# Performance work log

Hardware: AMD Instinct MI355X
Metric: run time of the kernel (lower is better)

Reference implementation:

```python
import jax, jax.numpy as jnp
import numpy as np
from jax import lax

TEMPERATURE = 0.5
MOMENTUM = 0.9
EPS = 1e-12  # F.normalize eps

B, D, K = 8192, 512, 16384


def _l2norm(x):
    # matches F.normalize(p=2): x / max(||x||, eps)
    n = jnp.sqrt(jnp.sum(x * x, axis=-1, keepdims=True))
    return x / jnp.maximum(n, EPS)


def setup_inputs() -> dict:
    key = jax.random.key(0)
    k1, k2, k3 = jax.random.split(key, 3)
    embeddings = jax.random.normal(k1, (B, D), dtype=jnp.float32)
    cluster_ids = jax.random.randint(k2, (B,), 0, K, dtype=jnp.int64)
    prototypes = jax.random.normal(k3, (K, D), dtype=jnp.float32)
    return {"embeddings": embeddings, "cluster_ids": cluster_ids, "prototypes": prototypes}


def reference(embeddings, cluster_ids, prototypes):
    emb_n = _l2norm(embeddings)            # [B, D]
    proto_n = _l2norm(prototypes)          # [K, D]
    sim = jnp.einsum('bd,kd->bk', emb_n, proto_n) / TEMPERATURE  # [B, K]

    pos = jnp.take_along_axis(sim, cluster_ids[:, None], axis=1)  # [B, 1]
    # mask out the positive column, then stable logsumexp over negatives
    is_pos = jnp.arange(sim.shape[1])[None, :] == cluster_ids[:, None]  # [B, K]
    neg = jnp.where(is_pos, -jnp.inf, sim)
    lse = jax.scipy.special.logsumexp(neg, axis=1, keepdims=True)       # [B, 1]
    loss = jnp.mean(-pos + lse)

    # serial momentum EMA update (order-dependent for duplicate cluster ids)
    def step(protos, xc):
        x, c = xc
        row = MOMENTUM * protos[c] + (1.0 - MOMENTUM) * x
        return protos.at[c].set(row), None

    new_protos, _ = lax.scan(step, prototypes, (embeddings, cluster_ids))
    return loss, new_protos
```

## Files before the change

kernel.cpp:

```cpp
#include <hip/hip_runtime.h>
#include <hip/hip_bf16.h>


#define B_N 8192
#define D_N 512
#define K_N 16384
#define INV_T 2.0f
#define MOM 0.9f

#define BM 128
#define BN 128
#define SPLIT 32
#define TILES ((K_N / SPLIT) / BN)
#define CHUNKS (D_N / 128)
#define CAP 64

typedef __attribute__((ext_vector_type(8))) int intx8;
typedef __attribute__((ext_vector_type(16))) float floatx16;

__device__ __forceinline__ void gl_lds16(const void* g, void* lds) {
    __builtin_amdgcn_global_load_lds(
        (const __attribute__((address_space(1))) void*)g,
        (__attribute__((address_space(3))) void*)lds, 16, 0, 0);
}

__global__ void head_kernel(const float* __restrict__ emb, const float* __restrict__ pro,
                            const int* __restrict__ cid,
                            unsigned char* __restrict__ embq, unsigned char* __restrict__ proq,
                            float* __restrict__ rowpos, float* __restrict__ rowsum,
                            float* __restrict__ out, int* __restrict__ cnt) {
    int bx = blockIdx.x;
    int t = threadIdx.x;
    int lane = t & 63;
    if (bx < (B_N + K_N) / 4) {
        if (bx < 32) rowsum[bx * 256 + t] = 0.0f;
        if (bx == 32 && t == 0) out[0] = 0.0f;
        int row = bx * 4 + (t >> 6);
        const float* x;
        unsigned char* o;
        if (row < B_N) {
            x = emb + (size_t)row * D_N;
            o = embq + (size_t)row * D_N;
        } else {
            x = pro + (size_t)(row - B_N) * D_N;
            o = proq + (size_t)(row - B_N) * D_N;
        }
        const float4* xp = (const float4*)(x + lane * 8);
        float4 v0 = xp[0];
        float4 v1 = xp[1];
        float ss = v0.x * v0.x + v0.y * v0.y + v0.z * v0.z + v0.w * v0.w +
                   v1.x * v1.x + v1.y * v1.y + v1.z * v1.z + v1.w * v1.w;
        #pragma unroll
        for (int of = 32; of; of >>= 1) ss += __shfl_xor(ss, of);
        float sc = 16.0f / fmaxf(sqrtf(ss), 1e-12f);
        int w0 = 0, w1 = 0;
        w0 = __builtin_amdgcn_cvt_pk_fp8_f32(v0.x * sc, v0.y * sc, w0, false);
        w0 = __builtin_amdgcn_cvt_pk_fp8_f32(v0.z * sc, v0.w * sc, w0, true);
        w1 = __builtin_amdgcn_cvt_pk_fp8_f32(v1.x * sc, v1.y * sc, w1, false);
        w1 = __builtin_amdgcn_cvt_pk_fp8_f32(v1.z * sc, v1.w * sc, w1, true);
        int2 st = {w0, w1};
        *(int2*)(o + lane * 8) = st;
    } else {
        int pb = bx - (B_N + K_N) / 4;
        if (t < 8) cnt[pb * 8 + t] = 0;
        int b = pb * 4 + (t >> 6);
        int c = cid[b];
        const float4* ep = (const float4*)(emb + (size_t)b * D_N + lane * 8);
        const float4* pp = (const float4*)(pro + (size_t)c * D_N + lane * 8);
        float4 e0 = ep[0], e1 = ep[1], p0 = pp[0], p1 = pp[1];
        float dp = e0.x * p0.x + e0.y * p0.y + e0.z * p0.z + e0.w * p0.w +
                   e1.x * p1.x + e1.y * p1.y + e1.z * p1.z + e1.w * p1.w;
        float ee = e0.x * e0.x + e0.y * e0.y + e0.z * e0.z + e0.w * e0.w +
                   e1.x * e1.x + e1.y * e1.y + e1.z * e1.z + e1.w * e1.w;
        float qq = p0.x * p0.x + p0.y * p0.y + p0.z * p0.z + p0.w * p0.w +
                   p1.x * p1.x + p1.y * p1.y + p1.z * p1.z + p1.w * p1.w;
        #pragma unroll
        for (int o = 32; o; o >>= 1) {
            dp += __shfl_xor(dp, o);
            ee += __shfl_xor(ee, o);
            qq += __shfl_xor(qq, o);
        }
        if (lane == 0)
            rowpos[b] = INV_T * dp / (fmaxf(sqrtf(ee), 1e-12f) * fmaxf(sqrtf(qq), 1e-12f));
    }
}

__global__ __launch_bounds__(256) void flash_kernel(const unsigned char* __restrict__ embq,
                                                    const unsigned char* __restrict__ proq,
                                                    float* __restrict__ rowsum_g) {
    __shared__ __align__(16) unsigned char As[BM * 128];
    __shared__ __align__(16) unsigned char Bs[BN * 128];
    const int t = threadIdx.x;
    const int w = t >> 6, lane = t & 63;
    const int m = lane & 31, q2 = lane >> 5;
    const int wm = w >> 1, wn = w & 1;
    const int rowBase = blockIdx.x * BM;
    const int nBegin = blockIdx.y * (K_N / SPLIT);

    const int e = (m >> 1) & 3;
    const int s0 = (((q2 << 1) | 0) ^ e) << 4;
    const int s1 = s0 ^ 16;
    const unsigned char* aR = &As[(wm * 64 + m) * 64];
    const unsigned char* bR = &Bs[(wn * 64 + m) * 64];

    const unsigned char* aSrcP[4];
    const unsigned char* bSrcP[4];
    #pragma unroll
    for (int p = 0; p < 4; p++) {
        int f = p * 256 + t;
        int r = (f >> 2) & 127;
        int h = f >> 9;
        int g = (f & 3) ^ ((r >> 1) & 3);
        aSrcP[p] = embq + (size_t)(rowBase + r) * D_N + h * 64 + g * 16;
        bSrcP[p] = proq + (size_t)(nBegin + r) * D_N + h * 64 + g * 16;
    }

    float rowsum[32];
    #pragma unroll
    for (int i = 0; i < 32; i++) rowsum[i] = 0.0f;

    #pragma unroll
    for (int p = 0; p < 4; p++) {
        gl_lds16(aSrcP[p], &As[p * 4096 + w * 1024]);
        gl_lds16(bSrcP[p], &Bs[p * 4096 + w * 1024]);
    }

    for (int tile = 0; tile < TILES; tile++) {
        floatx16 acc[2][2];
        #pragma unroll
        for (int mt = 0; mt < 2; mt++)
            #pragma unroll
            for (int nt = 0; nt < 2; nt++)
                #pragma unroll
                for (int r = 0; r < 16; r++) acc[mt][nt][r] = 0.0f;
        #pragma unroll
        for (int ch = 0; ch < CHUNKS; ch++) {
            __syncthreads();
            intx8 af[2][2], bf[2][2];
            #pragma unroll
            for (int mt = 0; mt < 2; mt++)
                #pragma unroll
                for (int h = 0; h < 2; h++) {
                    int4 lo = *(const int4*)(aR + mt * 2048 + h * 8192 + s0);
                    int4 hi = *(const int4*)(aR + mt * 2048 + h * 8192 + s1);
                    intx8 v = {lo.x, lo.y, lo.z, lo.w, hi.x, hi.y, hi.z, hi.w};
                    af[mt][h] = v;
                }
            #pragma unroll
            for (int nt = 0; nt < 2; nt++)
                #pragma unroll
                for (int h = 0; h < 2; h++) {
                    int4 lo = *(const int4*)(bR + nt * 2048 + h * 8192 + s0);
                    int4 hi = *(const int4*)(bR + nt * 2048 + h * 8192 + s1);
                    intx8 v = {lo.x, lo.y, lo.z, lo.w, hi.x, hi.y, hi.z, hi.w};
                    bf[nt][h] = v;
                }
            __syncthreads();
            if (ch + 1 < CHUNKS) {
                #pragma unroll
                for (int p = 0; p < 4; p++) {
                    gl_lds16(aSrcP[p] + (ch + 1) * 128, &As[p * 4096 + w * 1024]);
                    gl_lds16(bSrcP[p] + (ch + 1) * 128, &Bs[p * 4096 + w * 1024]);
                }
            } else if (tile + 1 < TILES) {
                #pragma unroll
                for (int p = 0; p < 4; p++) {
                    gl_lds16(aSrcP[p], &As[p * 4096 + w * 1024]);
                    gl_lds16(bSrcP[p] + (size_t)BN * D_N, &Bs[p * 4096 + w * 1024]);
                }
            }
            #pragma unroll
            for (int mt = 0; mt < 2; mt++)
                #pragma unroll
                for (int nt = 0; nt < 2; nt++)
                    #pragma unroll
                    for (int h = 0; h < 2; h++)
                        acc[mt][nt] = __builtin_amdgcn_mfma_scale_f32_32x32x64_f8f6f4(
                            af[mt][h], bf[nt][h], acc[mt][nt], 0, 0, 0, 0x7F7F7F7F, 0,
                            0x7F7F7F7F);
        }
        #pragma unroll
        for (int p = 0; p < 4; p++) bSrcP[p] += (size_t)BN * D_N;
        #pragma unroll
        for (int mt = 0; mt < 2; mt++)
            #pragma unroll
            for (int nt = 0; nt < 2; nt++)
                #pragma unroll
                for (int r = 0; r < 16; r++)
                    rowsum[mt * 16 + r] += __expf(acc[mt][nt][r] * (INV_T / 256.0f));
    }
    #pragma unroll
    for (int i = 0; i < 32; i++) {
        #pragma unroll
        for (int o = 1; o < 32; o <<= 1) rowsum[i] += __shfl_xor(rowsum[i], o);
    }
    if (m == 0) {
        #pragma unroll
        for (int mt = 0; mt < 2; mt++)
            #pragma unroll
            for (int r = 0; r < 16; r++)
                atomicAdd(&rowsum_g[rowBase + wm * 64 + mt * 32 + (r & 3) + 8 * (r >> 2) +
                                    4 * q2],
                          rowsum[mt * 16 + r]);
    }
}

__global__ void loss_kernel(const float* __restrict__ rowsum, const float* __restrict__ rowpos,
                            float* __restrict__ out) {
    __shared__ float red[256];
    int t = threadIdx.x;
    int b = blockIdx.x * 256 + t;
    float p = rowpos[b];
    red[t] = logf(rowsum[b] - __expf(p)) - p;
    __syncthreads();
    for (int o = 128; o; o >>= 1) {
        if (t < o) red[t] += red[t + o];
        __syncthreads();
    }
    if (t == 0) atomicAdd(out, red[0] * (1.0f / (float)B_N));
}

__global__ void ema_count(const int* __restrict__ cid, int* __restrict__ cnt,
                          int* __restrict__ bucket) {
    int b = blockIdx.x * 256 + threadIdx.x;
    int c = cid[b];
    int slot = atomicAdd(&cnt[c], 1);
    if (slot < CAP) bucket[c * CAP + slot] = b;
}

__global__ void ema_apply(const float* __restrict__ emb, const float* __restrict__ pro,
                          const int* __restrict__ cnt, const int* __restrict__ bucket,
                          float* __restrict__ outp) {
    int k = blockIdx.x * 4 + (threadIdx.x >> 6);
    int lane = threadIdx.x & 63;
    int n = cnt[k];
    n = n < CAP ? n : CAP;
    const float4* pp = (const float4*)(pro + (size_t)k * D_N + lane * 8);
    float4 a0 = pp[0], a1 = pp[1];
    int myb = (lane < n) ? bucket[k * CAP + lane] : 0x7fffffff;
    for (int i = 0; i < n; i++) {
        int m = myb;
        #pragma unroll
        for (int o = 1; o < 64; o <<= 1) {
            int v = __shfl_xor(m, o);
            m = v < m ? v : m;
        }
        const float4* ep = (const float4*)(emb + (size_t)m * D_N + lane * 8);
        float4 e0 = ep[0], e1 = ep[1];
        a0.x = MOM * a0.x + (1.0f - MOM) * e0.x;
        a0.y = MOM * a0.y + (1.0f - MOM) * e0.y;
        a0.z = MOM * a0.z + (1.0f - MOM) * e0.z;
        a0.w = MOM * a0.w + (1.0f - MOM) * e0.w;
        a1.x = MOM * a1.x + (1.0f - MOM) * e1.x;
        a1.y = MOM * a1.y + (1.0f - MOM) * e1.y;
        a1.z = MOM * a1.z + (1.0f - MOM) * e1.z;
        a1.w = MOM * a1.w + (1.0f - MOM) * e1.w;
        if (myb == m) myb = 0x7fffffff;
    }
    float4* op = (float4*)(outp + (size_t)k * D_N + lane * 8);
    op[0] = a0;
    op[1] = a1;
}

extern "C" void kernel_launch(void* const* d_in, const int* in_sizes, int n_in,
                              void* d_out, int out_size, void* d_ws, size_t ws_size,
                              hipStream_t stream) {
    const float* emb = (const float*)d_in[0];
    const int* cid = (const int*)d_in[1];
    const float* pro = (const float*)d_in[2];
    float* out = (float*)d_out;

    char* ws = (char*)d_ws;
    unsigned char* embq = (unsigned char*)ws;
    unsigned char* proq = (unsigned char*)(ws + 4194304);
    float* rowsum = (float*)(ws + 12582912);
    float* rowpos = (float*)(ws + 12615680);
    int* cnt = (int*)(ws + 12648448);
    int* bucket = (int*)(ws + 12713984);

    head_kernel<<<(B_N + K_N) / 4 + B_N / 4, 256, 0, stream>>>(emb, pro, cid, embq, proq,
                                                               rowpos, rowsum, out, cnt);
    ema_count<<<B_N / 256, 256, 0, stream>>>(cid, cnt, bucket);
    flash_kernel<<<dim3(B_N / BM, SPLIT), 256, 0, stream>>>(embq, proq, rowsum);
    loss_kernel<<<B_N / 256, 256, 0, stream>>>(rowsum, rowpos, out);
    ema_apply<<<K_N / 4, 256, 0, stream>>>(emb, pro, cnt, bucket, out + 1);
}
```

Baseline: 214.6 us.

## Restructure FP8 flash GEMM with 16x16x128 MFMA, register B operands, and merged tail kernel

The similarity GEMM kernel is reorganised. The row tile doubles to 256, A tiles are double-buffered in LDS, and B (prototype) fragments are loaded straight from global memory into registers instead of staged through LDS. It switches from 32x32x64 to 16x16x128 scaled FP8 MFMA with an 8x4 accumulator tile per wave. The loss reduction and EMA apply kernels are merged into one launch to save a kernel launch. Risks: B is no longer shared through LDS, so global traffic rises and loads may be uncoalesced, and the larger accumulator set raises register pressure.

```diff
diff --git a/kernel.cpp b/kernel.cpp
--- a/kernel.cpp
+++ b/kernel.cpp
@@ -8,15 +8,13 @@
 #define INV_T 2.0f
 #define MOM 0.9f
 
-#define BM 128
+#define BM 256
 #define BN 128
 #define SPLIT 32
-#define TILES ((K_N / SPLIT) / BN)
-#define CHUNKS (D_N / 128)
 #define CAP 64
 
 typedef __attribute__((ext_vector_type(8))) int intx8;
-typedef __attribute__((ext_vector_type(16))) float floatx16;
+typedef __attribute__((ext_vector_type(4))) float floatx4;
 
 __device__ __forceinline__ void gl_lds16(const void* g, void* lds) {
     __builtin_amdgcn_global_load_lds(
@@ -88,136 +86,107 @@
 __global__ __launch_bounds__(256) void flash_kernel(const unsigned char* __restrict__ embq,
                                                     const unsigned char* __restrict__ proq,
                                                     float* __restrict__ rowsum_g) {
-    __shared__ __align__(16) unsigned char As[BM * 128];
-    __shared__ __align__(16) unsigned char Bs[BN * 128];
+    __shared__ __align__(16) unsigned char As[2][BM * 128];
     const int t = threadIdx.x;
     const int w = t >> 6, lane = t & 63;
-    const int m = lane & 31, q2 = lane >> 5;
+    const int quad = lane >> 4, lcol = lane & 15;
     const int wm = w >> 1, wn = w & 1;
     const int rowBase = blockIdx.x * BM;
     const int nBegin = blockIdx.y * (K_N / SPLIT);
 
-    const int e = (m >> 1) & 3;
-    const int s0 = (((q2 << 1) | 0) ^ e) << 4;
+    const int srow = t >> 3;
+    const int sG = ((t & 7) ^ (srow & 7)) << 4;
+    const unsigned char* aSrc = embq + (size_t)(rowBase + srow) * D_N + sG;
+
+    const int s0 = ((quad << 1) ^ (lcol & 7)) << 4;
     const int s1 = s0 ^ 16;
-    const unsigned char* aR = &As[(wm * 64 + m) * 64];
-    const unsigned char* bR = &Bs[(wn * 64 + m) * 64];
-
-    const unsigned char* aSrcP[4];
-    const unsigned char* bSrcP[4];
-    #pragma unroll
-    for (int p = 0; p < 4; p++) {
-        int f = p * 256 + t;
-        int r = (f >> 2) & 127;
-        int h = f >> 9;
-        int g = (f & 3) ^ ((r >> 1) & 3);
-        aSrcP[p] = embq + (size_t)(rowBase + r) * D_N + h * 64 + g * 16;
-        bSrcP[p] = proq + (size_t)(nBegin + r) * D_N + h * 64 + g * 16;
-    }
+    const int aRow = (wm * 128 + lcol) * 128;
+
+    const unsigned char* bPtr = proq + (size_t)(nBegin + wn * 64 + lcol) * D_N + quad * 32;
 
     float rowsum[32];
     #pragma unroll
     for (int i = 0; i < 32; i++) rowsum[i] = 0.0f;
 
     #pragma unroll
-    for (int p = 0; p < 4; p++) {
-        gl_lds16(aSrcP[p], &As[p * 4096 + w * 1024]);
-        gl_lds16(bSrcP[p], &Bs[p * 4096 + w * 1024]);
-    }
-
-    for (int tile = 0; tile < TILES; tile++) {
-        floatx16 acc[2][2];
-        #pragma unroll
-        for (int mt = 0; mt < 2; mt++)
-            #pragma unroll
-            for (int nt = 0; nt < 2; nt++)
-                #pragma unroll
-                for (int r = 0; r < 16; r++) acc[mt][nt][r] = 0.0f;
-        #pragma unroll
-        for (int ch = 0; ch < CHUNKS; ch++) {
+    for (int p = 0; p < 8; p++)
+        gl_lds16(aSrc + p * 32 * D_N, &As[0][p * 4096 + w * 1024]);
+
+    #pragma unroll
+    for (int tile = 0; tile < 4; tile++) {
+        floatx4 acc[8][4];
+        #pragma unroll
+        for (int mt = 0; mt < 8; mt++)
+            #pragma unroll
+            for (int nt = 0; nt < 4; nt++) {
+                floatx4 z = {0.0f, 0.0f, 0.0f, 0.0f};
+                acc[mt][nt] = z;
+            }
+        #pragma unroll
+        for (int ch = 0; ch < 4; ch++) {
+            const int buf = ch & 1;
             __syncthreads();
-            intx8 af[2][2], bf[2][2];
-            #pragma unroll
-            for (int mt = 0; mt < 2; mt++)
-                #pragma unroll
-                for (int h = 0; h < 2; h++) {
-                    int4 lo = *(const int4*)(aR + mt * 2048 + h * 8192 + s0);
-                    int4 hi = *(const int4*)(aR + mt * 2048 + h * 8192 + s1);
-                    intx8 v = {lo.x, lo.y, lo.z, lo.w, hi.x, hi.y, hi.z, hi.w};
-                    af[mt][h] = v;
+            intx8 bf[4];
+            #pragma unroll
+            for (int nt = 0; nt < 4; nt++) {
+                const unsigned char* q =
+                    bPtr + tile * (BN * D_N) + nt * (16 * D_N) + ch * 128;
+                int4 lo = *(const int4*)(q);
+                int4 hi = *(const int4*)(q + 16);
+                intx8 v = {lo.x, lo.y, lo.z, lo.w, hi.x, hi.y, hi.z, hi.w};
+                bf[nt] = v;
+            }
+            if (ch < 3) {
+                #pragma unroll
+                for (int p = 0; p < 8; p++)
+                    gl_lds16(aSrc + p * 32 * D_N + (ch + 1) * 128,
+                             &As[buf ^ 1][p * 4096 + w * 1024]);
+            } else if (tile < 3) {
+                #pragma unroll
+                for (int p = 0; p < 8; p++)
+                    gl_lds16(aSrc + p * 32 * D_N, &As[buf ^ 1][p * 4096 + w * 1024]);
+            }
+            #pragma unroll
+            for (int ph = 0; ph < 4; ph++) {
+                const unsigned char* a0 = &As[buf][aRow + (2 * ph) * 2048];
+                const unsigned char* a1 = &As[buf][aRow + (2 * ph + 1) * 2048];
+                int4 l0 = *(const int4*)(a0 + s0);
+                int4 h0 = *(const int4*)(a0 + s1);
+                int4 l1 = *(const int4*)(a1 + s0);
+                int4 h1 = *(const int4*)(a1 + s1);
+                intx8 af0 = {l0.x, l0.y, l0.z, l0.w, h0.x, h0.y, h0.z, h0.w};
+                intx8 af1 = {l1.x, l1.y, l1.z, l1.w, h1.x, h1.y, h1.z, h1.w};
+                #pragma unroll
+                for (int nt = 0; nt < 4; nt++) {
+                    acc[2 * ph][nt] = __builtin_amdgcn_mfma_scale_f32_16x16x128_f8f6f4(
+                        af0, bf[nt], acc[2 * ph][nt], 0, 0, 0, 0x7F7F7F7F, 0, 0x7F7F7F7F);
+                    acc[2 * ph + 1][nt] = __builtin_amdgcn_mfma_scale_f32_16x16x128_f8f6f4(
+                        af1, bf[nt], acc[2 * ph + 1][nt], 0, 0, 0, 0x7F7F7F7F, 0,
+                        0x7F7F7F7F);
                 }
-            #pragma unroll
-            for (int nt = 0; nt < 2; nt++)
-                #pragma unroll
-                for (int h = 0; h < 2; h++) {
-                    int4 lo = *(const int4*)(bR + nt * 2048 + h * 8192 + s0);
-                    int4 hi = *(const int4*)(bR + nt * 2048 + h * 8192 + s1);
-                    intx8 v = {lo.x, lo.y, lo.z, lo.w, hi.x, hi.y, hi.z, hi.w};
-                    bf[nt][h] = v;
-                }
-            __syncthreads();
-            if (ch + 1 < CHUNKS) {
-                #pragma unroll
-                for (int p = 0; p < 4; p++) {
-                    gl_lds16(aSrcP[p] + (ch + 1) * 128, &As[p * 4096 + w * 1024]);
-                    gl_lds16(bSrcP[p] + (ch + 1) * 128, &Bs[p * 4096 + w * 1024]);
-                }
-            } else if (tile + 1 < TILES) {
-                #pragma unroll
-                for (int p = 0; p < 4; p++) {
-                    gl_lds16(aSrcP[p], &As[p * 4096 + w * 1024]);
-                    gl_lds16(bSrcP[p] + (size_t)BN * D_N, &Bs[p * 4096 + w * 1024]);
-                }
-            }
-            #pragma unroll
-            for (int mt = 0; mt < 2; mt++)
-                #pragma unroll
-                for (int nt = 0; nt < 2; nt++)
-                    #pragma unroll
-                    for (int h = 0; h < 2; h++)
-                        acc[mt][nt] = __builtin_amdgcn_mfma_scale_f32_32x32x64_f8f6f4(
-                            af[mt][h], bf[nt][h], acc[mt][nt], 0, 0, 0, 0x7F7F7F7F, 0,
-                            0x7F7F7F7F);
-        }
-        #pragma unroll
-        for (int p = 0; p < 4; p++) bSrcP[p] += (size_t)BN * D_N;
-        #pragma unroll
-        for (int mt = 0; mt < 2; mt++)
-            #pragma unroll
-            for (int nt = 0; nt < 2; nt++)
-                #pragma unroll
-                for (int r = 0; r < 16; r++)
-                    rowsum[mt * 16 + r] += __expf(acc[mt][nt][r] * (INV_T / 256.0f));
+            }
+        }
+        #pragma unroll
+        for (int mt = 0; mt < 8; mt++)
+            #pragma unroll
+            for (int nt = 0; nt < 4; nt++)
+                #pragma unroll
+                for (int r = 0; r < 4; r++)
+                    rowsum[mt * 4 + r] += __expf(acc[mt][nt][r] * (INV_T / 256.0f));
     }
     #pragma unroll
     for (int i = 0; i < 32; i++) {
         #pragma unroll
-        for (int o = 1; o < 32; o <<= 1) rowsum[i] += __shfl_xor(rowsum[i], o);
-    }
-    if (m == 0) {
-        #pragma unroll
-        for (int mt = 0; mt < 2; mt++)
-            #pragma unroll
-            for (int r = 0; r < 16; r++)
-                atomicAdd(&rowsum_g[rowBase + wm * 64 + mt * 32 + (r & 3) + 8 * (r >> 2) +
-                                    4 * q2],
-                          rowsum[mt * 16 + r]);
-    }
-}
-
-__global__ void loss_kernel(const float* __restrict__ rowsum, const float* __restrict__ rowpos,
-                            float* __restrict__ out) {
-    __shared__ float red[256];
-    int t = threadIdx.x;
-    int b = blockIdx.x * 256 + t;
-    float p = rowpos[b];
-    red[t] = logf(rowsum[b] - __expf(p)) - p;
-    __syncthreads();
-    for (int o = 128; o; o >>= 1) {
-        if (t < o) red[t] += red[t + o];
-        __syncthreads();
-    }
-    if (t == 0) atomicAdd(out, red[0] * (1.0f / (float)B_N));
+        for (int o = 1; o < 16; o <<= 1) rowsum[i] += __shfl_xor(rowsum[i], o);
+    }
+    if (lcol == 0) {
+        #pragma unroll
+        for (int mt = 0; mt < 8; mt++)
+            #pragma unroll
+            for (int r = 0; r < 4; r++)
+                atomicAdd(&rowsum_g[rowBase + wm * 128 + mt * 16 + quad * 4 + r],
+                          rowsum[mt * 4 + r]);
+    }
 }
 
 __global__ void ema_count(const int* __restrict__ cid, int* __restrict__ cnt,
@@ -228,11 +197,27 @@
     if (slot < CAP) bucket[c * CAP + slot] = b;
 }
 
-__global__ void ema_apply(const float* __restrict__ emb, const float* __restrict__ pro,
-                          const int* __restrict__ cnt, const int* __restrict__ bucket,
-                          float* __restrict__ outp) {
-    int k = blockIdx.x * 4 + (threadIdx.x >> 6);
-    int lane = threadIdx.x & 63;
+__global__ void tail_kernel(const float* __restrict__ rowsum, const float* __restrict__ rowpos,
+                            float* __restrict__ out, const float* __restrict__ emb,
+                            const float* __restrict__ pro, const int* __restrict__ cnt,
+                            const int* __restrict__ bucket, float* __restrict__ outp) {
+    int bx = blockIdx.x;
+    int t = threadIdx.x;
+    if (bx < 32) {
+        __shared__ float red[256];
+        int b = bx * 256 + t;
+        float p = rowpos[b];
+        red[t] = logf(rowsum[b] - __expf(p)) - p;
+        __syncthreads();
+        for (int o = 128; o; o >>= 1) {
+            if (t < o) red[t] += red[t + o];
+            __syncthreads();
+        }
+        if (t == 0) atomicAdd(out, red[0] * (1.0f / (float)B_N));
+        return;
+    }
+    int k = (bx - 32) * 4 + (t >> 6);
+    int lane = t & 63;
     int n = cnt[k];
     n = n < CAP ? n : CAP;
     const float4* pp = (const float4*)(pro + (size_t)k * D_N + lane * 8);
@@ -282,6 +267,6 @@
                                                                rowpos, rowsum, out, cnt);
     ema_count<<<B_N / 256, 256, 0, stream>>>(cid, cnt, bucket);
     flash_kernel<<<dim3(B_N / BM, SPLIT), 256, 0, stream>>>(embq, proq, rowsum);
-    loss_kernel<<<B_N / 256, 256, 0, stream>>>(rowsum, rowpos, out);
-    ema_apply<<<K_N / 4, 256, 0, stream>>>(emb, pro, cnt, bucket, out + 1);
-}
+    tail_kernel<<<32 + K_N / 4, 256, 0, stream>>>(rowsum, rowpos, out, emb, pro, cnt,
+                                                  bucket, out + 1);
+}
```

New measurement: 269.0 us. 1.25x slower.
